# Kernel tuning notes

Hardware: AMD Instinct MI355X
Metric: run time of the kernel (lower is better)

## Reference

```python
import jax, jax.numpy as jnp
import numpy as np

DIM = 5120
NUM_HEADS = 40
HEAD_DIM = DIM // NUM_HEADS
EPS = 1e-6


def rms_norm(x, g):
    # RMSNorm over last dim in fp32 for stability
    xf = x.astype(jnp.float32)
    inv = jax.lax.rsqrt(jnp.mean(xf * xf, axis=-1, keepdims=True) + EPS)
    return (xf * inv).astype(x.dtype) * g


def setup_inputs() -> dict:
    key = jax.random.key(0)
    ks = jax.random.split(key, 12)
    B, S, L = 1, 4096, 512
    inp = {
        "hidden_cond": jax.random.normal(ks[0], (B, S, DIM), jnp.float32),
        "hidden_uncond": jax.random.normal(ks[1], (B, S, DIM), jnp.float32),
        "context_cond": jax.random.normal(ks[2], (B, L, DIM), jnp.float32),
        "context_uncond": jax.random.normal(ks[3], (B, L, DIM), jnp.float32),
        # parameters (torch nn.Linear: y = x @ W.T + b)
        "Wq": jax.random.normal(ks[4], (DIM, DIM), jnp.float32) * (DIM ** -0.5),
        "bq": jnp.zeros((DIM,), jnp.float32),
        "Wkv": jax.random.normal(ks[5], (2 * DIM, DIM), jnp.float32) * (DIM ** -0.5),
        "bkv": jnp.zeros((2 * DIM,), jnp.float32),
        "gq": jnp.ones((DIM,), jnp.float32),
        "gk": jnp.ones((DIM,), jnp.float32),
        "Wo": jax.random.normal(ks[6], (DIM, DIM), jnp.float32) * (DIM ** -0.5),
        "bo": jnp.zeros((DIM,), jnp.float32),
    }
    return inp


def reference(hidden_cond, hidden_uncond, context_cond, context_uncond,
              Wq, bq, Wkv, bkv, gq, gk, Wo, bo):
    H, Dh = NUM_HEADS, HEAD_DIM
    scale = Dh ** -0.5

    hidden = jnp.concatenate([hidden_cond, hidden_uncond], axis=0)   # [2B, S, D]
    context = jnp.concatenate([context_cond, context_uncond], axis=0)  # [2B, L, D]
    CB, S, D = hidden.shape
    L = context.shape[1]

    q = hidden @ Wq.T + bq                    # [2B, S, D]
    q = rms_norm(q, gq)
    q = q.reshape(CB, S, H, Dh).transpose(0, 2, 1, 3)  # [2B, H, S, Dh]

    kv = context @ Wkv.T + bkv                # [2B, L, 2D]
    kv = kv.reshape(CB, L, 2, H, Dh).transpose(2, 0, 3, 1, 4)  # [2,2B,H,L,Dh]
    k, v = kv[0], kv[1]

    k_flat = k.transpose(0, 2, 1, 3).reshape(CB, L, D)
    k_flat = rms_norm(k_flat, gk)
    k = k_flat.reshape(CB, L, H, Dh).transpose(0, 2, 1, 3)  # [2B, H, L, Dh]

    attn = jnp.einsum('bhsd,bhld->bhsl', q, k) * scale
    attn = jax.nn.softmax(attn.astype(jnp.float32), axis=-1).astype(q.dtype)
    out = jnp.einsum('bhsl,bhld->bhsd', attn, v)            # [2B, H, S, Dh]
    out = out.transpose(0, 2, 1, 3).reshape(CB, S, D)
    out = out @ Wo.T + bo

    out_cond, out_uncond = jnp.split(out, 2, axis=0)
    return (out_cond, out_uncond)
```

## Files before the change

### kernel.cpp

```cpp
#include <hip/hip_runtime.h>
#include <hip/hip_bf16.h>
#include <cstdint>
#include <cstddef>

#define DIM 5120
#define NH 40
#define HD 128
#define S_LEN 4096
#define L_LEN 512
#define CBATCH 2
#define MQ (CBATCH*S_LEN)
#define ML (CBATCH*L_LEN)

typedef unsigned short ushort_t;
typedef __bf16 bf16x8 __attribute__((ext_vector_type(8)));
typedef float f32x4 __attribute__((ext_vector_type(4)));
typedef float f32x16 __attribute__((ext_vector_type(16)));

__device__ __forceinline__ ushort_t f2bf(float f) {
  union { float f; unsigned u; } c; c.f = f;
  unsigned r = c.u + 0x7fffu + ((c.u >> 16) & 1u);
  return (ushort_t)(r >> 16);
}

__device__ __forceinline__ void load_lds16(const void* g, void* l) {
  __builtin_amdgcn_global_load_lds(
      (const __attribute__((address_space(1))) void*)g,
      (__attribute__((address_space(3))) void*)l, 16, 0, 0);
}

#define CB0 (S_LEN*DIM/4)
#define CB1 (2*CB0)
#define CB2 (CB1 + L_LEN*DIM/4)
#define CB3 (CB2 + L_LEN*DIM/4)
#define CB4 (CB3 + DIM*DIM/4)
#define CB5 (CB4 + 2*DIM*DIM/4)
__global__ __launch_bounds__(256) void cvt_all(const float* __restrict__ hc,
                                               const float* __restrict__ hu,
                                               const float* __restrict__ cc,
                                               const float* __restrict__ cu,
                                               const float* __restrict__ wq,
                                               const float* __restrict__ wkv,
                                               ushort_t* __restrict__ hbf,
                                               ushort_t* __restrict__ cbf,
                                               ushort_t* __restrict__ wqb,
                                               ushort_t* __restrict__ wkvb) {
  const int stride = gridDim.x * 256;
  for (int i = blockIdx.x * 256 + threadIdx.x; i < CB5; i += stride) {
    const float* src;
    ushort_t* dst;
    if (i < CB1) {
      src = (i < CB0) ? hc + 4ull * (size_t)i : hu + 4ull * (size_t)(i - CB0);
      dst = hbf + 4ull * (size_t)i;
    } else if (i < CB3) {
      src = (i < CB2) ? cc + 4ull * (size_t)(i - CB1) : cu + 4ull * (size_t)(i - CB2);
      dst = cbf + 4ull * (size_t)(i - CB1);
    } else if (i < CB4) {
      src = wq + 4ull * (size_t)(i - CB3);
      dst = wqb + 4ull * (size_t)(i - CB3);
    } else {
      src = wkv + 4ull * (size_t)(i - CB4);
      dst = wkvb + 4ull * (size_t)(i - CB4);
    }
    float4 v = *(const float4*)src;
    ushort4 o;
    o.x = f2bf(v.x); o.y = f2bf(v.y); o.z = f2bf(v.z); o.w = f2bf(v.w);
    *(ushort4*)dst = o;
  }
}

template <int OUT_F32>
__device__ __forceinline__ void gemm_core(const ushort_t* __restrict__ Ab,
                                          const ushort_t* __restrict__ Bb,
                                          const float* __restrict__ bias,
                                          void* __restrict__ Cout,
                                          int N, size_t m0, size_t n0,
                                          char* ldsc) {
  const int tid = threadIdx.x;
  const int lane = tid & 63, w = tid >> 6;
  const int g = lane >> 4, c = lane & 15;
  const int wm = w >> 2, wn = w & 3;
  constexpr int K = DIM;
  constexpr int NT = K >> 6;

  const int srow = tid >> 2;
  const int sgq  = (tid & 3) ^ (((tid >> 5) & 1) << 1);
  const size_t rb0 = (size_t)srow * K + (size_t)sgq * 8;
  const size_t rb1 = rb0 + (size_t)128 * K;
  const int d0 = tid * 16;

  int offA[8], offB[4];
#pragma unroll
  for (int m = 0; m < 8; ++m) {
    int row = wm * 128 + m * 16 + c;
    offA[m] = row * 64 + ((g * 16) ^ ((row & 8) << 2));
  }
#pragma unroll
  for (int n = 0; n < 4; ++n) {
    int row = wn * 64 + n * 16 + c;
    offB[n] = row * 64 + ((g * 16) ^ ((row & 8) << 2));
  }

  auto STAGE = [&](int tIdx, int j, int dOff) {
    const size_t kof = (size_t)tIdx * 64 + (size_t)((j >> 1) << 5);
    const ushort_t* gsrc = ((j & 1) ? Ab : Bb) + kof;
    char* db = ldsc + dOff;
    load_lds16(gsrc + rb0, db + d0);
    load_lds16(gsrc + rb1, db + 8192 + d0);
  };
  auto nx = [](int x) { return (x + 16384 == 147456) ? 0 : x + 16384; };

  f32x4 acc[8][4] = {};

#pragma unroll
  for (int h = 0; h < 8; ++h) STAGE(h >> 2, h & 3, h * 16384);
  asm volatile("s_waitcnt vmcnt(8)" ::: "memory");
  __builtin_amdgcn_s_barrier();

  int rd = 0;
  int sOff = 131072;
  for (int t = 0; t < NT; ++t) {
    const int r0 = rd, r1 = nx(r0), r2 = nx(r1), r3 = nx(r2);
    bf16x8 a[4], a2[4], b[4];
#pragma unroll
    for (int m = 0; m < 4; ++m) a[m] = *(const bf16x8*)(ldsc + r1 + offA[m]);
#pragma unroll
    for (int n = 0; n < 4; ++n) b[n] = *(const bf16x8*)(ldsc + r0 + offB[n]);
    if (t < NT - 2) { STAGE(t + 2, 0, sOff); sOff = nx(sOff); }
    __builtin_amdgcn_s_barrier();
    asm volatile("s_waitcnt lgkmcnt(0)" ::: "memory");
    __builtin_amdgcn_sched_barrier(0);
    __builtin_amdgcn_s_setprio(1);
#pragma unroll
    for (int m = 0; m < 4; ++m)
#pragma unroll
      for (int n = 0; n < 4; ++n)
        acc[m][n] = __builtin_amdgcn_mfma_f32_16x16x32_bf16(a[m], b[n], acc[m][n], 0, 0, 0);
    __builtin_amdgcn_s_setprio(0);
    __builtin_amdgcn_s_barrier();
#pragma unroll
    for (int m = 0; m < 4; ++m) a2[m] = *(const bf16x8*)(ldsc + r1 + offA[4 + m]);
    if (t < NT - 2) { STAGE(t + 2, 1, sOff); sOff = nx(sOff); }
    __builtin_amdgcn_s_barrier();
    asm volatile("s_waitcnt lgkmcnt(0)" ::: "memory");
    __builtin_amdgcn_sched_barrier(0);
    __builtin_amdgcn_s_setprio(1);
#pragma unroll
    for (int m = 0; m < 4; ++m)
#pragma unroll
      for (int n = 0; n < 4; ++n)
        acc[4 + m][n] = __builtin_amdgcn_mfma_f32_16x16x32_bf16(a2[m], b[n], acc[4 + m][n], 0, 0, 0);
    __builtin_amdgcn_s_setprio(0);
    __builtin_amdgcn_s_barrier();
#pragma unroll
    for (int m = 0; m < 4; ++m) a[m] = *(const bf16x8*)(ldsc + r3 + offA[m]);
#pragma unroll
    for (int n = 0; n < 4; ++n) b[n] = *(const bf16x8*)(ldsc + r2 + offB[n]);
    if (t < NT - 2) { STAGE(t + 2, 2, sOff); sOff = nx(sOff); }
    __builtin_amdgcn_s_barrier();
    asm volatile("s_waitcnt lgkmcnt(0)" ::: "memory");
    __builtin_amdgcn_sched_barrier(0);
    __builtin_amdgcn_s_setprio(1);
#pragma unroll
    for (int m = 0; m < 4; ++m)
#pragma unroll
      for (int n = 0; n < 4; ++n)
        acc[m][n] = __builtin_amdgcn_mfma_f32_16x16x32_bf16(a[m], b[n], acc[m][n], 0, 0, 0);
    __builtin_amdgcn_s_setprio(0);
    __builtin_amdgcn_s_barrier();
#pragma unroll
    for (int m = 0; m < 4; ++m) a2[m] = *(const bf16x8*)(ldsc + r3 + offA[4 + m]);
    if (t < NT - 2) { STAGE(t + 2, 3, sOff); sOff = nx(sOff); }
    __builtin_amdgcn_s_barrier();
    asm volatile("s_waitcnt lgkmcnt(0)" ::: "memory");
    __builtin_amdgcn_sched_barrier(0);
    __builtin_amdgcn_s_setprio(1);
#pragma unroll
    for (int m = 0; m < 4; ++m)
#pragma unroll
      for (int n = 0; n < 4; ++n)
        acc[4 + m][n] = __builtin_amdgcn_mfma_f32_16x16x32_bf16(a2[m], b[n], acc[4 + m][n], 0, 0, 0);
    __builtin_amdgcn_s_setprio(0);
    if (t < NT - 2)       asm volatile("s_waitcnt vmcnt(6)" ::: "memory");
    else if (t == NT - 2) asm volatile("s_waitcnt vmcnt(0)" ::: "memory");
    __builtin_amdgcn_s_barrier();
    rd = nx(r3);
  }

#pragma unroll
  for (int m = 0; m < 8; ++m) {
#pragma unroll
    for (int n = 0; n < 4; ++n) {
      size_t gm = m0 + wm * 128 + m * 16 + g * 4;
      size_t gn = n0 + wn * 64 + n * 16 + c;
      float bn = bias[gn];
#pragma unroll
      for (int r = 0; r < 4; ++r) {
        float v = acc[m][n][r] + bn;
        if (OUT_F32) ((float*)Cout)[(gm + r) * (size_t)N + gn] = v;
        else         ((ushort_t*)Cout)[(gm + r) * (size_t)N + gn] = f2bf(v);
      }
    }
  }
}

__global__ __launch_bounds__(512, 2) void gemm_fused_qkv(
    const ushort_t* __restrict__ hbf, const ushort_t* __restrict__ wq,
    const ushort_t* __restrict__ cbf, const ushort_t* __restrict__ wkv,
    const float* __restrict__ bq, const float* __restrict__ bkv,
    ushort_t* __restrict__ qb, ushort_t* __restrict__ kvb) {
  __shared__ ushort_t lds[73728];
  char* ldsc = (char*)lds;
  int bid = blockIdx.x;
  bid = (bid & 7) * 96 + (bid >> 3);
  if (bid < 640) {
    const int tm = bid / 20, tn = bid % 20;
    const size_t m0 = (size_t)tm * 256, n0 = (size_t)tn * 256;
    gemm_core<0>(hbf + m0 * DIM, wq + n0 * DIM, bq, qb, DIM, m0, n0, ldsc);
  } else {
    const int e = bid - 640;
    const int tm = e >> 5, tn = e & 31;
    const size_t m0 = (size_t)tm * 256, n0 = (size_t)tn * 256;
    gemm_core<0>(cbf + m0 * DIM, wkv + n0 * DIM, bkv, kvb, 2 * DIM, m0, n0, ldsc);
  }
}

__global__ __launch_bounds__(512, 2) void gemm_out(
    const ushort_t* __restrict__ A, const ushort_t* __restrict__ W,
    const float* __restrict__ bias, float* __restrict__ C) {
  __shared__ ushort_t lds[73728];
  char* ldsc = (char*)lds;
  int bid = blockIdx.x;
  bid = (bid & 7) * 80 + (bid >> 3);
  const int tm = bid / 20, tn = bid % 20;
  const size_t m0 = (size_t)tm * 256, n0 = (size_t)tn * 256;
  gemm_core<1>(A + m0 * DIM, W + n0 * DIM, bias, C, DIM, m0, n0, ldsc);
}

__global__ __launch_bounds__(256) void kv_tail(const ushort_t* __restrict__ A,
                                               const ushort_t* __restrict__ W,
                                               const float* __restrict__ bias,
                                               ushort_t* __restrict__ Cout,
                                               const float* __restrict__ wo,
                                               ushort_t* __restrict__ wob) {
  constexpr int K = DIM;
  const int tid = threadIdx.x;
  if (blockIdx.x >= 128) {
    const int nblk = gridDim.x - 128;
    const int stride = nblk * 256;
    for (int i = (blockIdx.x - 128) * 256 + tid; i < DIM * DIM / 4; i += stride) {
      float4 v = *(const float4*)(wo + 4ull * (size_t)i);
      ushort4 o;
      o.x = f2bf(v.x); o.y = f2bf(v.y); o.z = f2bf(v.z); o.w = f2bf(v.w);
      *(ushort4*)(wob + 4ull * (size_t)i) = o;
    }
    return;
  }
  __shared__ ushort_t sA[128 * 32];
  __shared__ ushort_t sB[128 * 32];
  const int w = tid >> 6, lane = tid & 63;
  const int g = lane >> 4, c = lane & 15;
  int bid = blockIdx.x;
  bid = (bid & 7) * 16 + (bid >> 3);
  const int tm = bid / 16, tn = bid % 16;
  const size_t m0 = (size_t)tm * 128, n0 = (size_t)tn * 128;
  const int wr = (w >> 1) * 64, wc = (w & 1) * 64;

  f32x4 acc[4][4] = {};

  const ushort_t* Abase = A + m0 * (size_t)K;
  const ushort_t* Bbase = W + n0 * (size_t)K;

  for (int k0 = 0; k0 < K; k0 += 32) {
    __syncthreads();
#pragma unroll
    for (int i = 0; i < 2; ++i) {
      int gid = i * 256 + tid;
      int row = gid >> 2, colE = (gid & 3) << 3;
      load_lds16(Abase + (size_t)row * K + k0 + colE, sA + i * 2048 + w * 512);
      load_lds16(Bbase + (size_t)row * K + k0 + colE, sB + i * 2048 + w * 512);
    }
    __syncthreads();
    bf16x8 a[4], b[4];
#pragma unroll
    for (int m = 0; m < 4; ++m)
      a[m] = *(const bf16x8*)(sA + (wr + m * 16 + c) * 32 + g * 8);
#pragma unroll
    for (int n = 0; n < 4; ++n)
      b[n] = *(const bf16x8*)(sB + (wc + n * 16 + c) * 32 + g * 8);
#pragma unroll
    for (int m = 0; m < 4; ++m)
#pragma unroll
      for (int n = 0; n < 4; ++n)
        acc[m][n] = __builtin_amdgcn_mfma_f32_16x16x32_bf16(a[m], b[n], acc[m][n], 0, 0, 0);
  }

#pragma unroll
  for (int m = 0; m < 4; ++m) {
#pragma unroll
    for (int n = 0; n < 4; ++n) {
      size_t gm = m0 + wr + m * 16 + g * 4;
      size_t gn = n0 + wc + n * 16 + c;
      float bn = bias[gn];
#pragma unroll
      for (int r = 0; r < 4; ++r) {
        float v = acc[m][n][r] + bn;
        Cout[(gm + r) * (size_t)(2 * DIM) + gn] = f2bf(v);
      }
    }
  }
}

__global__ __launch_bounds__(256) void norm_and_transpose(
    ushort_t* __restrict__ qx, ushort_t* __restrict__ kvx,
    const float* __restrict__ gq, const float* __restrict__ gk,
    float qscale, ushort_t* __restrict__ vt) {
  const int tid = threadIdx.x;
  if (blockIdx.x >= MQ + ML) {
    const int e = blockIdx.x - (MQ + ML);
    const int bh = e / 16, b = bh / NH, h = bh % NH;
    const int l0 = (e % 16) * 32;
    const ushort_t* src = kvx + (size_t)b * L_LEN * (2 * DIM) + DIM + (size_t)h * HD;
    ushort_t* dst = vt + (size_t)bh * HD * L_LEN;
    __shared__ ushort_t tile[32][HD + 16];
#pragma unroll
    for (int i = 0; i < 2; ++i) {
      int gid = i * 256 + tid;
      int r = gid >> 4, ce = (gid & 15) << 3;
      *(bf16x8*)(&tile[r][ce]) = *(const bf16x8*)(src + (size_t)(l0 + r) * (2 * DIM) + ce);
    }
    __syncthreads();
#pragma unroll
    for (int i = 0; i < 2; ++i) {
      int gid = i * 256 + tid;
      int d = gid >> 2, le = (gid & 3) << 3;
      bf16x8 v;
#pragma unroll
      for (int j = 0; j < 8; ++j) v[j] = *(__bf16*)&tile[le + j][d];
      *(bf16x8*)(dst + (size_t)d * L_LEN + l0 + le) = v;
    }
    return;
  }
  const int row = blockIdx.x;
  ushort_t* p;
  const float* gw;
  float oscale;
  if (row < MQ) { p = qx + (size_t)row * DIM; gw = gq; oscale = qscale; }
  else { p = kvx + (size_t)(row - MQ) * (2 * DIM); gw = gk; oscale = 1.0f; }
  const int nch = DIM >> 3;
  float ss = 0.f;
  for (int ci = tid; ci < nch; ci += 256) {
    bf16x8 v = *(const bf16x8*)(p + ci * 8);
#pragma unroll
    for (int j = 0; j < 8; ++j) { float f = (float)v[j]; ss += f * f; }
  }
#pragma unroll
  for (int off = 1; off < 64; off <<= 1) ss += __shfl_xor(ss, off);
  __shared__ float sred[4];
  if ((tid & 63) == 0) sred[tid >> 6] = ss;
  __syncthreads();
  float tot = sred[0] + sred[1] + sred[2] + sred[3];
  float inv = rsqrtf(tot / (float)DIM + 1e-6f) * oscale;
  for (int ci = tid; ci < nch; ci += 256) {
    bf16x8 v = *(const bf16x8*)(p + ci * 8);
    bf16x8 ov;
#pragma unroll
    for (int j = 0; j < 8; ++j) {
      float f = (float)v[j];
      ushort_t ob = f2bf(f * inv * gw[ci * 8 + j]);
      ov[j] = *(__bf16*)&ob;
    }
    *(bf16x8*)(p + ci * 8) = ov;
  }
}

__global__ __launch_bounds__(256) void attn_fwd(const ushort_t* __restrict__ q,
                                                const ushort_t* __restrict__ kv,
                                                const ushort_t* __restrict__ vt,
                                                ushort_t* __restrict__ out) {
  const int bh = blockIdx.y, b = bh / NH, h = bh % NH;
  const int tid = threadIdx.x, w = tid >> 6, lane = tid & 63;
  const int lq = lane & 31, hi = lane >> 5;
  const int qr0 = blockIdx.x * 128 + w * 32;

  __shared__ ushort_t sK[2][4096];
  __shared__ ushort_t sV[2][4096];

  const int skl = tid >> 3, skc = tid & 7;
  const ushort_t* kgsrc = kv + ((size_t)b * L_LEN + skl) * (2 * DIM)
                             + (size_t)h * HD + skc * 16;
  ushort_t* kd0 = &sK[0][(skc * 2) * 256 + skl * 8];
  ushort_t* kd1 = &sK[0][(skc * 2 + 1) * 256 + skl * 8];
  const int svd = tid >> 1, svh = tid & 1;
  const ushort_t* vgsrc = vt + (size_t)bh * HD * L_LEN + (size_t)svd * L_LEN + svh * 16;
  ushort_t* vd0 = &sV[0][(svh * 2) * 1024 + svd * 8];
  ushort_t* vd1 = &sV[0][(svh * 2 + 1) * 1024 + svd * 8];

  const ushort_t* qrow = q + ((size_t)b * S_LEN + qr0 + lq) * DIM + (size_t)h * HD + hi * 8;
  bf16x8 qf[8];
#pragma unroll
  for (int ks = 0; ks < 8; ++ks) qf[ks] = *(const bf16x8*)(qrow + ks * 16);

  f32x16 o[4];
#pragma unroll
  for (int ch = 0; ch < 4; ++ch) o[ch] = 0.f;
  float m = -1e30f, lsum = 0.f;

  {
    uint4 ka = *(const uint4*)kgsrc;
    uint4 kb = *(const uint4*)(kgsrc + 8);
    uint4 va = *(const uint4*)vgsrc;
    uint4 vb = *(const uint4*)(vgsrc + 8);
    *(uint4*)kd0 = ka; *(uint4*)kd1 = kb;
    *(uint4*)vd0 = va; *(uint4*)vd1 = vb;
  }
  __syncthreads();

  const int NT = L_LEN / 32;
  int buf = 0;
  for (int t = 0; t < NT; ++t) {
    uint4 ka, kb, va, vb;
    if (t + 1 < NT) {
      const ushort_t* kg = kgsrc + (size_t)(t + 1) * 32 * (2 * DIM);
      const ushort_t* vg = vgsrc + (t + 1) * 32;
      ka = *(const uint4*)kg; kb = *(const uint4*)(kg + 8);
      va = *(const uint4*)vg; vb = *(const uint4*)(vg + 8);
    }

    const ushort_t* kbuf = sK[buf];
    const ushort_t* vbuf = sV[buf];

    f32x16 sv = 0.f;
    __builtin_amdgcn_s_setprio(1);
#pragma unroll
    for (int ks = 0; ks < 8; ++ks) {
      bf16x8 kf = *(const bf16x8*)(kbuf + (ks * 2 + hi) * 256 + lq * 8);
      sv = __builtin_amdgcn_mfma_f32_32x32x16_bf16(kf, qf[ks], sv, 0, 0, 0);
    }
    __builtin_amdgcn_s_setprio(0);
    float pm = fmaxf(fmaxf(fmaxf(sv[0], sv[1]), fmaxf(sv[2], sv[3])),
                     fmaxf(fmaxf(sv[4], sv[5]), fmaxf(sv[6], sv[7])));
    pm = fmaxf(pm, fmaxf(fmaxf(fmaxf(sv[8], sv[9]), fmaxf(sv[10], sv[11])),
                         fmaxf(fmaxf(sv[12], sv[13]), fmaxf(sv[14], sv[15]))));
    pm = fmaxf(pm, __shfl_xor(pm, 32));
    if (__ballot(pm > m + 8.0f)) {
      float mn = fmaxf(m, pm);
      float al = __builtin_amdgcn_exp2f(m - mn);
      lsum *= al;
      m = mn;
#pragma unroll
      for (int r = 0; r < 16; ++r) {
        float ar = __shfl(al, (r & 3) + 8 * (r >> 2) + 4 * hi);
        o[0][r] *= ar; o[1][r] *= ar; o[2][r] *= ar; o[3][r] *= ar;
      }
    }
    float p[16]; float ls = 0.f;
#pragma unroll
    for (int r = 0; r < 16; ++r) { p[r] = __builtin_amdgcn_exp2f(sv[r] - m); ls += p[r]; }
    ls += __shfl_xor(ls, 32);
    lsum += ls;
    bf16x8 pa[2];
#pragma unroll
    for (int ks = 0; ks < 2; ++ks) {
      unsigned w0 = (unsigned)f2bf(p[8 * ks + 0]) | ((unsigned)f2bf(p[8 * ks + 1]) << 16);
      unsigned w1 = (unsigned)f2bf(p[8 * ks + 2]) | ((unsigned)f2bf(p[8 * ks + 3]) << 16);
      unsigned w2 = (unsigned)f2bf(p[8 * ks + 4]) | ((unsigned)f2bf(p[8 * ks + 5]) << 16);
      unsigned w3 = (unsigned)f2bf(p[8 * ks + 6]) | ((unsigned)f2bf(p[8 * ks + 7]) << 16);
      unsigned e0 = __shfl_xor((int)w0, 32), e1 = __shfl_xor((int)w1, 32);
      unsigned e2 = __shfl_xor((int)w2, 32), e3 = __shfl_xor((int)w3, 32);
      unsigned d0 = hi ? e2 : w0, d1 = hi ? e3 : w1;
      unsigned d2 = hi ? w2 : e0, d3 = hi ? w3 : e1;
      unsigned tmp[4] = {d0, d1, d2, d3};
      pa[ks] = *(const bf16x8*)tmp;
    }
    __builtin_amdgcn_s_setprio(1);
#pragma unroll
    for (int ch = 0; ch < 4; ++ch) {
#pragma unroll
      for (int ks = 0; ks < 2; ++ks) {
        bf16x8 vf = *(const bf16x8*)(vbuf + (ks * 2 + hi) * 1024 + (ch * 32 + lq) * 8);
        o[ch] = __builtin_amdgcn_mfma_f32_32x32x16_bf16(pa[ks], vf, o[ch], 0, 0, 0);
      }
    }
    __builtin_amdgcn_s_setprio(0);

    if (t + 1 < NT) {
      const int nb = buf ^ 1;
      *(uint4*)(kd0 + nb * 4096) = ka; *(uint4*)(kd1 + nb * 4096) = kb;
      *(uint4*)(vd0 + nb * 4096) = va; *(uint4*)(vd1 + nb * 4096) = vb;
    }
    __syncthreads();
    buf ^= 1;
  }

  float inv[16];
#pragma unroll
  for (int r = 0; r < 16; ++r) {
    float lr = __shfl(lsum, (r & 3) + 8 * (r >> 2) + 4 * hi);
    inv[r] = 1.0f / lr;
  }
  ushort_t* ob = out + ((size_t)b * S_LEN + qr0) * DIM + (size_t)h * HD;
#pragma unroll
  for (int ch = 0; ch < 4; ++ch)
#pragma unroll
    for (int r = 0; r < 16; ++r) {
      int row = (r & 3) + 8 * (r >> 2) + 4 * hi;
      ob[(size_t)row * DIM + ch * 32 + lq] = f2bf(o[ch][r] * inv[r]);
    }
}

extern "C" void kernel_launch(void* const* d_in, const int* in_sizes, int n_in,
                              void* d_out, int out_size, void* d_ws, size_t ws_size,
                              hipStream_t stream) {
  (void)in_sizes; (void)n_in; (void)out_size; (void)ws_size;
  const float* hidden_c = (const float*)d_in[0];
  const float* hidden_u = (const float*)d_in[1];
  const float* ctx_c    = (const float*)d_in[2];
  const float* ctx_u    = (const float*)d_in[3];
  const float* Wq  = (const float*)d_in[4];
  const float* bq  = (const float*)d_in[5];
  const float* Wkv = (const float*)d_in[6];
  const float* bkv = (const float*)d_in[7];
  const float* gq  = (const float*)d_in[8];
  const float* gk  = (const float*)d_in[9];
  const float* Wo  = (const float*)d_in[10];
  const float* bo  = (const float*)d_in[11];

  char* ws = (char*)d_ws;
  size_t off = 0;
  auto alloc = [&](size_t bytes) {
    char* p = ws + off; off += (bytes + 255) & ~(size_t)255; return p;
  };
  ushort_t* hbf  = (ushort_t*)alloc((size_t)MQ * DIM * 2);
  ushort_t* cbf  = (ushort_t*)alloc((size_t)ML * DIM * 2);
  ushort_t* wqb  = (ushort_t*)alloc((size_t)DIM * DIM * 2);
  ushort_t* wkvb = (ushort_t*)alloc((size_t)2 * DIM * DIM * 2);
  ushort_t* kvb  = (ushort_t*)alloc((size_t)ML * 2 * DIM * 2);
  ushort_t* vtb  = (ushort_t*)alloc((size_t)CBATCH * NH * HD * L_LEN * 2);
  ushort_t* qb   = (ushort_t*)d_out;

  cvt_all<<<dim3(2048), dim3(256), 0, stream>>>(
      hidden_c, hidden_u, ctx_c, ctx_u, Wq, Wkv, hbf, cbf, wqb, wkvb);

  gemm_fused_qkv<<<dim3(768), dim3(512), 0, stream>>>(
      hbf, wqb, cbf, wkvb, bq, bkv, qb, kvb);
  kv_tail<<<dim3(1152), dim3(256), 0, stream>>>(
      cbf, wkvb + (size_t)8192 * DIM, bkv + 8192, kvb + 8192, Wo, wqb);

  const float qscale = 0.08838834764831845f * 1.4426950408889634f;
  norm_and_transpose<<<dim3(MQ + ML + 16 * CBATCH * NH), dim3(256), 0, stream>>>(
      qb, kvb, gq, gk, qscale, vtb);

  attn_fwd<<<dim3(S_LEN / 128, CBATCH * NH), dim3(256), 0, stream>>>(qb, kvb, vtb, hbf);

  gemm_out<<<dim3(640), dim3(512), 0, stream>>>(hbf, wqb, bo, (float*)d_out);
}
```

Before: 1.376 ms.

## Shrink GEMM pipeline to one-ahead prefetch and fold KV tail into fused GEMM

The GEMM core's LDS ring drops from 9 to 5 stage slots (144 KB to 80 KB), so prefetch runs one K-tile ahead instead of two and each iteration waits for all outstanding loads. The fused QKV GEMM grid grows from 768 to 800 blocks so it covers the full 10240-wide KV projection, which removes the separate kv_tail kernel. The Wo conversion moves into a standalone cvt_wo kernel. This cuts LDS per block and removes the slower 128x128 tail GEMM, but it gives up load/compute overlap depth.

```diff
diff --git a/kernel.cpp b/kernel.cpp
--- a/kernel.cpp
+++ b/kernel.cpp
@@ -108,17 +108,17 @@
     load_lds16(gsrc + rb0, db + d0);
     load_lds16(gsrc + rb1, db + 8192 + d0);
   };
-  auto nx = [](int x) { return (x + 16384 == 147456) ? 0 : x + 16384; };
+  auto nx = [](int x) { return (x + 16384 == 81920) ? 0 : x + 16384; };
 
   f32x4 acc[8][4] = {};
 
 #pragma unroll
-  for (int h = 0; h < 8; ++h) STAGE(h >> 2, h & 3, h * 16384);
-  asm volatile("s_waitcnt vmcnt(8)" ::: "memory");
+  for (int h = 0; h < 4; ++h) STAGE(0, h, h * 16384);
+  asm volatile("s_waitcnt vmcnt(0)" ::: "memory");
   __builtin_amdgcn_s_barrier();
 
   int rd = 0;
-  int sOff = 131072;
+  int sOff = 65536;
   for (int t = 0; t < NT; ++t) {
     const int r0 = rd, r1 = nx(r0), r2 = nx(r1), r3 = nx(r2);
     bf16x8 a[4], a2[4], b[4];
@@ -126,7 +126,7 @@
     for (int m = 0; m < 4; ++m) a[m] = *(const bf16x8*)(ldsc + r1 + offA[m]);
 #pragma unroll
     for (int n = 0; n < 4; ++n) b[n] = *(const bf16x8*)(ldsc + r0 + offB[n]);
-    if (t < NT - 2) { STAGE(t + 2, 0, sOff); sOff = nx(sOff); }
+    if (t < NT - 1) { STAGE(t + 1, 0, sOff); sOff = nx(sOff); }
     __builtin_amdgcn_s_barrier();
     asm volatile("s_waitcnt lgkmcnt(0)" ::: "memory");
     __builtin_amdgcn_sched_barrier(0);
@@ -140,7 +140,7 @@
     __builtin_amdgcn_s_barrier();
 #pragma unroll
     for (int m = 0; m < 4; ++m) a2[m] = *(const bf16x8*)(ldsc + r1 + offA[4 + m]);
-    if (t < NT - 2) { STAGE(t + 2, 1, sOff); sOff = nx(sOff); }
+    if (t < NT - 1) { STAGE(t + 1, 1, sOff); sOff = nx(sOff); }
     __builtin_amdgcn_s_barrier();
     asm volatile("s_waitcnt lgkmcnt(0)" ::: "memory");
     __builtin_amdgcn_sched_barrier(0);
@@ -156,7 +156,7 @@
     for (int m = 0; m < 4; ++m) a[m] = *(const bf16x8*)(ldsc + r3 + offA[m]);
 #pragma unroll
     for (int n = 0; n < 4; ++n) b[n] = *(const bf16x8*)(ldsc + r2 + offB[n]);
-    if (t < NT - 2) { STAGE(t + 2, 2, sOff); sOff = nx(sOff); }
+    if (t < NT - 1) { STAGE(t + 1, 2, sOff); sOff = nx(sOff); }
     __builtin_amdgcn_s_barrier();
     asm volatile("s_waitcnt lgkmcnt(0)" ::: "memory");
     __builtin_amdgcn_sched_barrier(0);
@@ -170,7 +170,7 @@
     __builtin_amdgcn_s_barrier();
 #pragma unroll
     for (int m = 0; m < 4; ++m) a2[m] = *(const bf16x8*)(ldsc + r3 + offA[4 + m]);
-    if (t < NT - 2) { STAGE(t + 2, 3, sOff); sOff = nx(sOff); }
+    if (t < NT - 1) { STAGE(t + 1, 3, sOff); sOff = nx(sOff); }
     __builtin_amdgcn_s_barrier();
     asm volatile("s_waitcnt lgkmcnt(0)" ::: "memory");
     __builtin_amdgcn_sched_barrier(0);
@@ -181,8 +181,7 @@
       for (int n = 0; n < 4; ++n)
         acc[4 + m][n] = __builtin_amdgcn_mfma_f32_16x16x32_bf16(a2[m], b[n], acc[4 + m][n], 0, 0, 0);
     __builtin_amdgcn_s_setprio(0);
-    if (t < NT - 2)       asm volatile("s_waitcnt vmcnt(6)" ::: "memory");
-    else if (t == NT - 2) asm volatile("s_waitcnt vmcnt(0)" ::: "memory");
+    if (t < NT - 1) asm volatile("s_waitcnt vmcnt(0)" ::: "memory");
     __builtin_amdgcn_s_barrier();
     rd = nx(r3);
   }
@@ -209,17 +208,17 @@
     const ushort_t* __restrict__ cbf, const ushort_t* __restrict__ wkv,
     const float* __restrict__ bq, const float* __restrict__ bkv,
     ushort_t* __restrict__ qb, ushort_t* __restrict__ kvb) {
-  __shared__ ushort_t lds[73728];
+  __shared__ ushort_t lds[40960];
   char* ldsc = (char*)lds;
   int bid = blockIdx.x;
-  bid = (bid & 7) * 96 + (bid >> 3);
+  bid = (bid & 7) * 100 + (bid >> 3);
   if (bid < 640) {
     const int tm = bid / 20, tn = bid % 20;
     const size_t m0 = (size_t)tm * 256, n0 = (size_t)tn * 256;
     gemm_core<0>(hbf + m0 * DIM, wq + n0 * DIM, bq, qb, DIM, m0, n0, ldsc);
   } else {
     const int e = bid - 640;
-    const int tm = e >> 5, tn = e & 31;
+    const int tm = e / 40, tn = e % 40;
     const size_t m0 = (size_t)tm * 256, n0 = (size_t)tn * 256;
     gemm_core<0>(cbf + m0 * DIM, wkv + n0 * DIM, bkv, kvb, 2 * DIM, m0, n0, ldsc);
   }
@@ -228,7 +227,7 @@
 __global__ __launch_bounds__(512, 2) void gemm_out(
     const ushort_t* __restrict__ A, const ushort_t* __restrict__ W,
     const float* __restrict__ bias, float* __restrict__ C) {
-  __shared__ ushort_t lds[73728];
+  __shared__ ushort_t lds[40960];
   char* ldsc = (char*)lds;
   int bid = blockIdx.x;
   bid = (bid & 7) * 80 + (bid >> 3);
@@ -237,77 +236,14 @@
   gemm_core<1>(A + m0 * DIM, W + n0 * DIM, bias, C, DIM, m0, n0, ldsc);
 }
 
-__global__ __launch_bounds__(256) void kv_tail(const ushort_t* __restrict__ A,
-                                               const ushort_t* __restrict__ W,
-                                               const float* __restrict__ bias,
-                                               ushort_t* __restrict__ Cout,
-                                               const float* __restrict__ wo,
-                                               ushort_t* __restrict__ wob) {
-  constexpr int K = DIM;
-  const int tid = threadIdx.x;
-  if (blockIdx.x >= 128) {
-    const int nblk = gridDim.x - 128;
-    const int stride = nblk * 256;
-    for (int i = (blockIdx.x - 128) * 256 + tid; i < DIM * DIM / 4; i += stride) {
-      float4 v = *(const float4*)(wo + 4ull * (size_t)i);
-      ushort4 o;
-      o.x = f2bf(v.x); o.y = f2bf(v.y); o.z = f2bf(v.z); o.w = f2bf(v.w);
-      *(ushort4*)(wob + 4ull * (size_t)i) = o;
-    }
-    return;
-  }
-  __shared__ ushort_t sA[128 * 32];
-  __shared__ ushort_t sB[128 * 32];
-  const int w = tid >> 6, lane = tid & 63;
-  const int g = lane >> 4, c = lane & 15;
-  int bid = blockIdx.x;
-  bid = (bid & 7) * 16 + (bid >> 3);
-  const int tm = bid / 16, tn = bid % 16;
-  const size_t m0 = (size_t)tm * 128, n0 = (size_t)tn * 128;
-  const int wr = (w >> 1) * 64, wc = (w & 1) * 64;
-
-  f32x4 acc[4][4] = {};
-
-  const ushort_t* Abase = A + m0 * (size_t)K;
-  const ushort_t* Bbase = W + n0 * (size_t)K;
-
-  for (int k0 = 0; k0 < K; k0 += 32) {
-    __syncthreads();
-#pragma unroll
-    for (int i = 0; i < 2; ++i) {
-      int gid = i * 256 + tid;
-      int row = gid >> 2, colE = (gid & 3) << 3;
-      load_lds16(Abase + (size_t)row * K + k0 + colE, sA + i * 2048 + w * 512);
-      load_lds16(Bbase + (size_t)row * K + k0 + colE, sB + i * 2048 + w * 512);
-    }
-    __syncthreads();
-    bf16x8 a[4], b[4];
-#pragma unroll
-    for (int m = 0; m < 4; ++m)
-      a[m] = *(const bf16x8*)(sA + (wr + m * 16 + c) * 32 + g * 8);
-#pragma unroll
-    for (int n = 0; n < 4; ++n)
-      b[n] = *(const bf16x8*)(sB + (wc + n * 16 + c) * 32 + g * 8);
-#pragma unroll
-    for (int m = 0; m < 4; ++m)
-#pragma unroll
-      for (int n = 0; n < 4; ++n)
-        acc[m][n] = __builtin_amdgcn_mfma_f32_16x16x32_bf16(a[m], b[n], acc[m][n], 0, 0, 0);
-  }
-
-#pragma unroll
-  for (int m = 0; m < 4; ++m) {
-#pragma unroll
-    for (int n = 0; n < 4; ++n) {
-      size_t gm = m0 + wr + m * 16 + g * 4;
-      size_t gn = n0 + wc + n * 16 + c;
-      float bn = bias[gn];
-#pragma unroll
-      for (int r = 0; r < 4; ++r) {
-        float v = acc[m][n][r] + bn;
-        Cout[(gm + r) * (size_t)(2 * DIM) + gn] = f2bf(v);
-      }
-    }
+__global__ __launch_bounds__(256) void cvt_wo(const float* __restrict__ wo,
+                                              ushort_t* __restrict__ wob) {
+  const int stride = gridDim.x * 256;
+  for (int i = blockIdx.x * 256 + threadIdx.x; i < DIM * DIM / 4; i += stride) {
+    float4 v = *(const float4*)(wo + 4ull * (size_t)i);
+    ushort4 o;
+    o.x = f2bf(v.x); o.y = f2bf(v.y); o.z = f2bf(v.z); o.w = f2bf(v.w);
+    *(ushort4*)(wob + 4ull * (size_t)i) = o;
   }
 }
 
@@ -542,10 +478,9 @@
   cvt_all<<<dim3(2048), dim3(256), 0, stream>>>(
       hidden_c, hidden_u, ctx_c, ctx_u, Wq, Wkv, hbf, cbf, wqb, wkvb);
 
-  gemm_fused_qkv<<<dim3(768), dim3(512), 0, stream>>>(
+  gemm_fused_qkv<<<dim3(800), dim3(512), 0, stream>>>(
       hbf, wqb, cbf, wkvb, bq, bkv, qb, kvb);
-  kv_tail<<<dim3(1152), dim3(256), 0, stream>>>(
-      cbf, wkvb + (size_t)8192 * DIM, bkv + 8192, kvb + 8192, Wo, wqb);
+  cvt_wo<<<dim3(1024), dim3(256), 0, stream>>>(Wo, wqb);
 
   const float qscale = 0.08838834764831845f * 1.4426950408889634f;
   norm_and_transpose<<<dim3(MQ + ML + 16 * CBATCH * NH), dim3(256), 0, stream>>>(
```

Result: no change. 1.379 ms (+0.3%).
